# Optimization experiments

Hardware: AMD Instinct MI355X
Metric: run time of the kernel (lower is better)

The kernel has to match this reference:

```python
import jax, jax.numpy as jnp
import numpy as np

B, L, E, D, A = 256, 196, 2048, 1024, 512


def setup_inputs() -> dict:
    key = jax.random.key(0)
    ks = jax.random.split(key, 9)
    enc_scale = 1.0 / np.sqrt(E)
    dec_scale = 1.0 / np.sqrt(D)
    att_scale = 1.0 / np.sqrt(A)
    return {
        "encoder_out": jax.random.normal(ks[0], (B, L, E), dtype=jnp.float32),
        "decoder_hidden": jax.random.normal(ks[1], (B, D), dtype=jnp.float32),
        "mask1": jax.random.randint(ks[2], (B, L), 0, 2, dtype=jnp.int32),
        "We": jax.random.uniform(ks[3], (E, A), jnp.float32, -enc_scale, enc_scale),
        "be": jax.random.uniform(ks[4], (A,), jnp.float32, -enc_scale, enc_scale),
        "Wd": jax.random.uniform(ks[5], (D, A), jnp.float32, -dec_scale, dec_scale),
        "bd": jax.random.uniform(ks[6], (A,), jnp.float32, -dec_scale, dec_scale),
        "wf": jax.random.uniform(ks[7], (A,), jnp.float32, -att_scale, att_scale),
        "bf": jax.random.uniform(ks[8], (), jnp.float32, -att_scale, att_scale),
    }


def reference(encoder_out, decoder_hidden, mask1, We, be, Wd, bd, wf, bf):
    # att1: [B, L, A]; att2: [B, A]
    att1 = jnp.einsum('ble,ea->bla', encoder_out, We) + be
    att2 = jnp.einsum('bd,da->ba', decoder_hidden, Wd) + bd
    # scores: [B, L]
    att = jnp.einsum('bla,a->bl', jnp.tanh(att1 + att2[:, None, :]), wf) + bf
    att = jnp.where(mask1 == 0, jnp.float32(-1e9), att)
    alpha = jax.nn.softmax(att, axis=1)
    # weighted sum over regions: [B, E]
    awe = jnp.einsum('ble,bl->be', encoder_out, alpha)
    return (awe, alpha)
```

## Files before the change

### kernel.cpp

```cpp
#include <hip/hip_runtime.h>
#include <hip/hip_bf16.h>


#define B_ 256
#define L_ 196
#define E_ 2048
#define D_ 1024
#define A_ 512
#define M_TOT (B_ * L_)

typedef __attribute__((ext_vector_type(8))) short bf16x8;
typedef __attribute__((ext_vector_type(4))) float f32x4;

static __device__ __forceinline__ unsigned short f2bf(float f) {
    union { float f; unsigned u; } u{f};
    unsigned r = u.u + 0x7fffu + ((u.u >> 16) & 1u);
    return (unsigned short)(r >> 16);
}

static __device__ __forceinline__ void gload_lds16(const void* g, void* l) {
    __builtin_amdgcn_global_load_lds(
        (const __attribute__((address_space(1))) unsigned int*)g,
        (__attribute__((address_space(3))) unsigned int*)l, 16, 0, 0);
}

__global__ __launch_bounds__(256) void k_wepack(const float* __restrict__ We,
                                                unsigned short* __restrict__ WeP) {
    int i = blockIdx.x * 256 + threadIdx.x;
    int k = i >> 9, n = i & 511;
    int kb = k >> 5, kg = (k >> 3) & 3, e = k & 7;
    int kgE = kg ^ ((n >> 1) & 3);
    WeP[(kb << 14) + (n << 5) + (kgE << 3) + e] = f2bf(We[i]);
}

__global__ __launch_bounds__(256) void k_bias2(const float* __restrict__ dec,
                                               const float* __restrict__ Wd,
                                               const float* __restrict__ be,
                                               const float* __restrict__ bd,
                                               float* __restrict__ bias2) {
    int b = blockIdx.x, t = threadIdx.x;
    __shared__ float ds[D_];
    for (int i = t; i < D_; i += 256) ds[i] = dec[b * D_ + i];
    __syncthreads();
    for (int a0 = 0; a0 < A_; a0 += 256) {
        int a = a0 + t;
        float acc = 0.f;
        #pragma unroll 8
        for (int d = 0; d < D_; d++) acc += ds[d] * Wd[d * A_ + a];
        bias2[b * A_ + a] = acc + be[a] + bd[a];
    }
}

__global__ __launch_bounds__(512) void k_gemm_score(
        const float* __restrict__ enc,
        const unsigned short* __restrict__ WeP,
        const float* __restrict__ bias2,
        const float* __restrict__ wf,
        float* __restrict__ scores) {
    __shared__ __align__(16) unsigned short aL[2][64 * 32];
    __shared__ __align__(16) unsigned short bL[2][512 * 32];
    __shared__ float score_lds[64];

    const int tid = threadIdx.x;
    const int m0 = blockIdx.x * 64;
    const int lane = tid & 63;
    const int wid = tid >> 6;
    const int wm = wid >> 2, wn = wid & 3;
    const int kg = lane >> 4, lr = lane & 15;

    const int ar = tid >> 3, ak = (tid & 7) << 2;
    const float* aSrc = enc + (size_t)(m0 + ar) * E_ + ak;
    const int aoff = ar * 32 + (ak ^ (((ar >> 1) & 3) << 3));
    unsigned short* aDst[2] = { &aL[0][aoff], &aL[1][aoff] };

    const unsigned short* bSrcLane = WeP + (size_t)(wid * 512 + lane * 8);

    auto stageB = [&](int kb, int buf) {
        const unsigned short* s = bSrcLane + ((size_t)kb << 14);
        unsigned short* d = &bL[buf][wid * 512];
        #pragma unroll
        for (int i = 0; i < 4; i++)
            gload_lds16(s + i * 4096, d + i * 4096);
    };
    auto writeA = [&](const float4& v, int buf) {
        short4 p;
        p.x = (short)f2bf(v.x); p.y = (short)f2bf(v.y);
        p.z = (short)f2bf(v.z); p.w = (short)f2bf(v.w);
        *reinterpret_cast<short4*>(aDst[buf]) = p;
    };

    f32x4 acc[2][8];
    #pragma unroll
    for (int i = 0; i < 2; i++)
        #pragma unroll
        for (int j = 0; j < 8; j++) acc[i][j] = (f32x4){0.f, 0.f, 0.f, 0.f};

    auto computeTile = [&](int buf) {
        bf16x8 afr[2];
        #pragma unroll
        for (int i = 0; i < 2; i++) {
            int row = wm * 32 + i * 16 + lr;
            afr[i] = *reinterpret_cast<const bf16x8*>(
                &aL[buf][row * 32 + ((kg ^ ((row >> 1) & 3)) << 3)]);
        }
        bf16x8 bfr[8];
        #pragma unroll
        for (int j = 0; j < 8; j++) {
            int n = wn * 128 + j * 16 + lr;
            bfr[j] = *reinterpret_cast<const bf16x8*>(
                &bL[buf][n * 32 + ((kg ^ ((n >> 1) & 3)) << 3)]);
        }
        #pragma unroll
        for (int i = 0; i < 2; i++)
            #pragma unroll
            for (int j = 0; j < 8; j++)
                acc[i][j] = __builtin_amdgcn_mfma_f32_16x16x32_bf16(
                    afr[i], bfr[j], acc[i][j], 0, 0, 0);
    };

    stageB(0, 0);
    float4 avCur = *reinterpret_cast<const float4*>(aSrc);
    float4 avHold = *reinterpret_cast<const float4*>(aSrc + 32);
    writeA(avCur, 0);
    __syncthreads();

    int buf = 0;
    for (int t = 0; t < 63; t++) {
        float4 avNext = avHold;
        if (t + 2 < 64)
            avNext = *reinterpret_cast<const float4*>(aSrc + (t + 2) * 32);
        stageB(t + 1, buf ^ 1);
        computeTile(buf);
        writeA(avHold, buf ^ 1);
        __syncthreads();
        avHold = avNext;
        buf ^= 1;
    }
    computeTile(buf);

    if (tid < 64) score_lds[tid] = 0.f;
    __syncthreads();
    #pragma unroll
    for (int i = 0; i < 2; i++) {
        #pragma unroll
        for (int r = 0; r < 4; r++) {
            int R = wm * 32 + i * 16 + kg * 4 + r;
            int gm = m0 + R;
            int bg = gm / L_;
            float sum = 0.f;
            #pragma unroll
            for (int j = 0; j < 8; j++) {
                int C = wn * 128 + j * 16 + lr;
                float x = acc[i][j][r] + bias2[bg * A_ + C];
                float ex = __expf(2.f * x);
                float th = 1.f - 2.f * __builtin_amdgcn_rcpf(ex + 1.f);
                sum += wf[C] * th;
            }
            #pragma unroll
            for (int mk = 1; mk < 16; mk <<= 1) sum += __shfl_xor(sum, mk);
            if (lr == 0) atomicAdd(&score_lds[R], sum);
        }
    }
    __syncthreads();
    if (tid < 64) scores[m0 + tid] = score_lds[tid];
}

__global__ __launch_bounds__(256) void k_softmax(const float* __restrict__ scores,
                                                 const int* __restrict__ mask,
                                                 const float* __restrict__ bfp,
                                                 float* __restrict__ alpha) {
    int b = blockIdx.x, t = threadIdx.x;
    float bfv = bfp[0];
    float v = -INFINITY;
    if (t < L_) v = (mask[b * L_ + t] == 0) ? -1e9f : (scores[b * L_ + t] + bfv);
    __shared__ float redm[4], reds[4];
    float m = v;
    #pragma unroll
    for (int s = 1; s < 64; s <<= 1) m = fmaxf(m, __shfl_xor(m, s));
    int w = t >> 6;
    if ((t & 63) == 0) redm[w] = m;
    __syncthreads();
    m = fmaxf(fmaxf(redm[0], redm[1]), fmaxf(redm[2], redm[3]));
    float e = (t < L_) ? expf(v - m) : 0.f;
    float s = e;
    #pragma unroll
    for (int k = 1; k < 64; k <<= 1) s += __shfl_xor(s, k);
    if ((t & 63) == 0) reds[w] = s;
    __syncthreads();
    s = reds[0] + reds[1] + reds[2] + reds[3];
    if (t < L_) alpha[b * L_ + t] = e / s;
}

__global__ __launch_bounds__(256) void k_awe(const float* __restrict__ enc,
                                             const float* __restrict__ alpha,
                                             float* __restrict__ awe) {
    int b = blockIdx.y, ec = blockIdx.x, t = threadIdx.x;
    int g = t >> 6, lt = t & 63;
    __shared__ float al[L_];
    __shared__ float4 red[256];
    if (t < L_) al[t] = alpha[b * L_ + t];
    __syncthreads();
    int e0 = (ec << 8) + (lt << 2);
    const float* base = enc + (size_t)b * L_ * E_ + e0;
    float4 acc = {0.f, 0.f, 0.f, 0.f};
    int l0 = g * 49;
    #pragma unroll 7
    for (int l = l0; l < l0 + 49; l++) {
        float4 v = *reinterpret_cast<const float4*>(base + (size_t)l * E_);
        float a = al[l];
        acc.x += a * v.x; acc.y += a * v.y; acc.z += a * v.z; acc.w += a * v.w;
    }
    red[t] = acc;
    __syncthreads();
    if (t < 64) {
        float4 r0 = red[t], r1 = red[64 + t], r2 = red[128 + t], r3 = red[192 + t];
        float4 o;
        o.x = r0.x + r1.x + r2.x + r3.x;
        o.y = r0.y + r1.y + r2.y + r3.y;
        o.z = r0.z + r1.z + r2.z + r3.z;
        o.w = r0.w + r1.w + r2.w + r3.w;
        *reinterpret_cast<float4*>(awe + b * E_ + (ec << 8) + (t << 2)) = o;
    }
}

extern "C" void kernel_launch(void* const* d_in, const int* in_sizes, int n_in,
                              void* d_out, int out_size, void* d_ws, size_t ws_size,
                              hipStream_t stream) {
    const float* enc  = (const float*)d_in[0];
    const float* dec  = (const float*)d_in[1];
    const int*   mask = (const int*)d_in[2];
    const float* We   = (const float*)d_in[3];
    const float* be   = (const float*)d_in[4];
    const float* Wd   = (const float*)d_in[5];
    const float* bd   = (const float*)d_in[6];
    const float* wf   = (const float*)d_in[7];
    const float* bf   = (const float*)d_in[8];

    float* awe   = (float*)d_out;
    float* alpha = awe + (size_t)B_ * E_;

    char* ws = (char*)d_ws;
    unsigned short* WeP = (unsigned short*)ws;
    float* bias2  = (float*)(ws + (2u << 20));
    float* scores = (float*)(ws + (2u << 20) + (512u << 10));

    hipLaunchKernelGGL(k_wepack, dim3((E_ * A_) / 256), dim3(256), 0, stream, We, WeP);
    hipLaunchKernelGGL(k_bias2, dim3(B_), dim3(256), 0, stream, dec, Wd, be, bd, bias2);
    hipLaunchKernelGGL(k_gemm_score, dim3(M_TOT / 64), dim3(512), 0, stream,
                       enc, WeP, bias2, wf, scores);
    hipLaunchKernelGGL(k_softmax, dim3(B_), dim3(256), 0, stream, scores, mask, bf, alpha);
    hipLaunchKernelGGL(k_awe, dim3(8, B_), dim3(256), 0, stream, enc, alpha, awe);
}
```

Baseline: 486.6 us.

## Retile GEMM warps to 64x64, deepen A prefetch, use manual waitcnt barriers

Changes each warp's output tile from 32x128 to 64x64 so every warp covers all 64 rows, reducing B-fragment LDS reads per tile. Deepens the register prefetch of encoder rows to three stages and replaces __syncthreads with explicit s_waitcnt vmcnt/lgkmcnt plus s_barrier and sched_barriers, so the in-flight A load can stay outstanding across the barrier. Also adds a min-blocks hint of 4 to launch bounds, which tightens the register budget and may cause spills of the 64-register accumulator.

Result: faster. 395.6 us (-18.7%).

```diff
diff --git a/kernel.cpp b/kernel.cpp
--- a/kernel.cpp
+++ b/kernel.cpp
@@ -51,7 +51,7 @@
     }
 }
 
-__global__ __launch_bounds__(512) void k_gemm_score(
+__global__ __launch_bounds__(512, 4) void k_gemm_score(
         const float* __restrict__ enc,
         const unsigned short* __restrict__ WeP,
         const float* __restrict__ bias2,
@@ -65,13 +65,11 @@
     const int m0 = blockIdx.x * 64;
     const int lane = tid & 63;
     const int wid = tid >> 6;
-    const int wm = wid >> 2, wn = wid & 3;
     const int kg = lane >> 4, lr = lane & 15;
 
     const int ar = tid >> 3, ak = (tid & 7) << 2;
     const float* aSrc = enc + (size_t)(m0 + ar) * E_ + ak;
     const int aoff = ar * 32 + (ak ^ (((ar >> 1) & 3) << 3));
-    unsigned short* aDst[2] = { &aL[0][aoff], &aL[1][aoff] };
 
     const unsigned short* bSrcLane = WeP + (size_t)(wid * 512 + lane * 8);
 
@@ -86,54 +84,58 @@
         short4 p;
         p.x = (short)f2bf(v.x); p.y = (short)f2bf(v.y);
         p.z = (short)f2bf(v.z); p.w = (short)f2bf(v.w);
-        *reinterpret_cast<short4*>(aDst[buf]) = p;
+        *reinterpret_cast<short4*>(&aL[buf][aoff]) = p;
     };
 
-    f32x4 acc[2][8];
-    #pragma unroll
-    for (int i = 0; i < 2; i++)
-        #pragma unroll
-        for (int j = 0; j < 8; j++) acc[i][j] = (f32x4){0.f, 0.f, 0.f, 0.f};
+    f32x4 acc[4][4];
+    #pragma unroll
+    for (int i = 0; i < 4; i++)
+        #pragma unroll
+        for (int j = 0; j < 4; j++) acc[i][j] = (f32x4){0.f, 0.f, 0.f, 0.f};
 
     auto computeTile = [&](int buf) {
-        bf16x8 afr[2];
-        #pragma unroll
-        for (int i = 0; i < 2; i++) {
-            int row = wm * 32 + i * 16 + lr;
-            afr[i] = *reinterpret_cast<const bf16x8*>(
-                &aL[buf][row * 32 + ((kg ^ ((row >> 1) & 3)) << 3)]);
-        }
-        bf16x8 bfr[8];
-        #pragma unroll
-        for (int j = 0; j < 8; j++) {
-            int n = wn * 128 + j * 16 + lr;
+        bf16x8 bfr[4];
+        #pragma unroll
+        for (int j = 0; j < 4; j++) {
+            int n = wid * 64 + j * 16 + lr;
             bfr[j] = *reinterpret_cast<const bf16x8*>(
                 &bL[buf][n * 32 + ((kg ^ ((n >> 1) & 3)) << 3)]);
         }
         #pragma unroll
-        for (int i = 0; i < 2; i++)
+        for (int i = 0; i < 4; i++) {
+            int row = i * 16 + lr;
+            bf16x8 af = *reinterpret_cast<const bf16x8*>(
+                &aL[buf][row * 32 + ((kg ^ ((row >> 1) & 3)) << 3)]);
             #pragma unroll
-            for (int j = 0; j < 8; j++)
+            for (int j = 0; j < 4; j++)
                 acc[i][j] = __builtin_amdgcn_mfma_f32_16x16x32_bf16(
-                    afr[i], bfr[j], acc[i][j], 0, 0, 0);
+                    af, bfr[j], acc[i][j], 0, 0, 0);
+        }
     };
 
     stageB(0, 0);
-    float4 avCur = *reinterpret_cast<const float4*>(aSrc);
-    float4 avHold = *reinterpret_cast<const float4*>(aSrc + 32);
-    writeA(avCur, 0);
-    __syncthreads();
+    __builtin_amdgcn_sched_barrier(0);
+    float4 av0  = *reinterpret_cast<const float4*>(aSrc);
+    float4 avH1 = *reinterpret_cast<const float4*>(aSrc + 32);
+    float4 avH2 = *reinterpret_cast<const float4*>(aSrc + 64);
+    writeA(av0, 0);
+    asm volatile("s_waitcnt vmcnt(2) lgkmcnt(0)" ::: "memory");
+    __builtin_amdgcn_s_barrier();
+    __builtin_amdgcn_sched_barrier(0);
 
     int buf = 0;
     for (int t = 0; t < 63; t++) {
-        float4 avNext = avHold;
-        if (t + 2 < 64)
-            avNext = *reinterpret_cast<const float4*>(aSrc + (t + 2) * 32);
         stageB(t + 1, buf ^ 1);
+        __builtin_amdgcn_sched_barrier(0);
+        int tn = (t + 3 > 63) ? 63 : t + 3;
+        float4 avN = *reinterpret_cast<const float4*>(aSrc + tn * 32);
+        __builtin_amdgcn_sched_barrier(0);
         computeTile(buf);
-        writeA(avHold, buf ^ 1);
-        __syncthreads();
-        avHold = avNext;
+        writeA(avH1, buf ^ 1);
+        asm volatile("s_waitcnt vmcnt(1) lgkmcnt(0)" ::: "memory");
+        __builtin_amdgcn_s_barrier();
+        __builtin_amdgcn_sched_barrier(0);
+        avH1 = avH2; avH2 = avN;
         buf ^= 1;
     }
     computeTile(buf);
@@ -141,16 +143,16 @@
     if (tid < 64) score_lds[tid] = 0.f;
     __syncthreads();
     #pragma unroll
-    for (int i = 0; i < 2; i++) {
+    for (int i = 0; i < 4; i++) {
         #pragma unroll
         for (int r = 0; r < 4; r++) {
-            int R = wm * 32 + i * 16 + kg * 4 + r;
+            int R = i * 16 + kg * 4 + r;
             int gm = m0 + R;
             int bg = gm / L_;
             float sum = 0.f;
             #pragma unroll
-            for (int j = 0; j < 8; j++) {
-                int C = wn * 128 + j * 16 + lr;
+            for (int j = 0; j < 4; j++) {
+                int C = wid * 64 + j * 16 + lr;
                 float x = acc[i][j][r] + bias2[bg * A_ + C];
                 float ex = __expf(2.f * x);
                 float th = 1.f - 2.f * __builtin_amdgcn_rcpf(ex + 1.f);
```
